# Kernel optimization log

Hardware: AMD Instinct MI355X
Metric: run time of the kernel (lower is better)

The kernel has to match this reference:

```python
import jax, jax.numpy as jnp
import numpy as np

DIM = 4096
BATCH = 8192
LAYERS = int(np.log2(DIM))  # 12


def _butterfly_indices(dim):
    lefts, rights = [], []
    for l in range(int(np.log2(dim))):
        stride = 1 << l
        starts = np.arange(0, dim, 2 * stride)[:, None]
        offs = np.arange(stride)[None, :]
        left = (starts + offs).reshape(-1)
        lefts.append(left)
        rights.append(left + stride)
    return np.stack(lefts), np.stack(rights)  # (layers, dim//2)


def setup_inputs() -> dict:
    key = jax.random.key(0)
    kx, ka = jax.random.split(key)
    x = jax.random.normal(kx, (BATCH, DIM), dtype=jnp.float32)
    # angles ~ Uniform(-0.05, 0.05), one per pair per layer
    angles = jax.random.uniform(ka, (LAYERS, DIM // 2), dtype=jnp.float32,
                                minval=-0.05, maxval=0.05)
    li, ri = _butterfly_indices(DIM)
    left_idx = jnp.asarray(li, dtype=jnp.int64) if jax.config.jax_enable_x64 else jnp.asarray(li, dtype=jnp.int32)
    right_idx = jnp.asarray(ri, dtype=left_idx.dtype)
    return {"x": x, "angles": angles, "left_idx": left_idx, "right_idx": right_idx}


def reference(x, angles, left_idx, right_idx):
    # x: (B, D); angles/left_idx/right_idx: (layers, D//2)
    y = x
    for l in range(angles.shape[0]):  # fixed small loop over log2(D) layers
        c = jnp.cos(angles[l])  # (D//2,)
        s = jnp.sin(angles[l])
        xl = jnp.take(y, left_idx[l], axis=1)   # (B, D//2)
        xr = jnpp_take(y, right_idx[l]) if False else jnp.take(y, right_idx[l], axis=1)
        new_left = xl * c + xr * s
        new_right = -xl * s + xr * c
        # left/right indices partition [0, D), so the scatter fully overwrites y
        y = jnp.zeros_like(y).at[:, left_idx[l]].set(new_left).at[:, right_idx[l]].set(new_right)
    return y
```

## Files before the change

kernel.cpp:

```cpp
#include <hip/hip_runtime.h>
#include <cmath>


namespace {
constexpr int kDim = 4096;
constexpr int kBatch = 8192;
constexpr int kLayers = 12;
constexpr int kPairs = kDim / 2;
constexpr int kRowsPerBlock = 2;
constexpr int kThreads = 256;
constexpr int kLdsWords = kDim + 4 * (kDim / 64);
}

__device__ __forceinline__ int lds_pad(int i) { return i + ((i >> 6) << 2); }

__device__ __forceinline__ int slot_to_pair(int l, int t, int q) {
    const int m = l & 3;
    const int phase = l >> 2;
    const int j = ((q >> m) << (m + 1)) | (q & ((1 << m) - 1));
    int i;
    if (phase == 0)      i = 16 * t + j;
    else if (phase == 1) i = (t & 15) + 16 * j + 256 * (t >> 4);
    else                 i = t + 256 * j;
    const int s = 1 << l;
    return ((i >> (l + 1)) << l) | (i & (s - 1));
}

__global__ void bf_precompute_cs(const float* __restrict__ angles,
                                 float* __restrict__ cperm,
                                 float* __restrict__ sperm) {
    const int k = blockIdx.x * blockDim.x + threadIdx.x;
    if (k >= kLayers * kPairs) return;
    const int l = k >> 11;
    const int slot = k & 2047;
    const int t = slot >> 3;
    const int q = slot & 7;
    const int p = slot_to_pair(l, t, q);
    const float a = angles[l * kPairs + p];
    float sv, cv;
    sincosf(a, &sv, &cv);
    cperm[k] = cv;
    sperm[k] = sv;
}

template <int PHASE>
__device__ __forceinline__ void apply_phase(float (&v)[kRowsPerBlock][16], int t,
                                            const float* __restrict__ cperm,
                                            const float* __restrict__ sperm) {
#pragma unroll
    for (int m = 0; m < 4; ++m) {
        const int l = PHASE * 4 + m;
        const float4* cp = reinterpret_cast<const float4*>(cperm + l * kPairs + 8 * t);
        const float4* sp = reinterpret_cast<const float4*>(sperm + l * kPairs + 8 * t);
        const float4 c0 = cp[0], c1 = cp[1];
        const float4 s0 = sp[0], s1 = sp[1];
        const float c[8] = {c0.x, c0.y, c0.z, c0.w, c1.x, c1.y, c1.z, c1.w};
        const float s[8] = {s0.x, s0.y, s0.z, s0.w, s1.x, s1.y, s1.z, s1.w};
#pragma unroll
        for (int q = 0; q < 8; ++q) {
            const int j = ((q >> m) << (m + 1)) | (q & ((1 << m) - 1));
            const int jp = j + (1 << m);
#pragma unroll
            for (int r = 0; r < kRowsPerBlock; ++r) {
                const float xl = v[r][j], xr = v[r][jp];
                v[r][j]  = fmaf(xl, c[q],  xr * s[q]);
                v[r][jp] = fmaf(xr, c[q], -xl * s[q]);
            }
        }
    }
}

__global__ __launch_bounds__(kThreads, 4)
void bf_butterfly(const float* __restrict__ x,
                  const float* __restrict__ cperm,
                  const float* __restrict__ sperm,
                  float* __restrict__ out) {
    __shared__ float lds[kRowsPerBlock][kLdsWords];
    const int t = threadIdx.x;
    const int row0 = blockIdx.x * kRowsPerBlock;

    float v[kRowsPerBlock][16];

#pragma unroll
    for (int r = 0; r < kRowsPerBlock; ++r) {
        const float4* src = reinterpret_cast<const float4*>(
            x + (size_t)(row0 + r) * kDim + 16 * t);
#pragma unroll
        for (int k = 0; k < 4; ++k) {
            const float4 f = src[k];
            v[r][4 * k + 0] = f.x; v[r][4 * k + 1] = f.y;
            v[r][4 * k + 2] = f.z; v[r][4 * k + 3] = f.w;
        }
    }

    apply_phase<0>(v, t, cperm, sperm);

#pragma unroll
    for (int r = 0; r < kRowsPerBlock; ++r) {
#pragma unroll
        for (int k = 0; k < 4; ++k) {
            *reinterpret_cast<float4*>(&lds[r][lds_pad(16 * t + 4 * k)]) =
                make_float4(v[r][4 * k], v[r][4 * k + 1], v[r][4 * k + 2], v[r][4 * k + 3]);
        }
    }
    __syncthreads();
    const int low = t & 15, high = t >> 4;
#pragma unroll
    for (int r = 0; r < kRowsPerBlock; ++r) {
#pragma unroll
        for (int j = 0; j < 16; ++j) {
            v[r][j] = lds[r][lds_pad(low + 16 * j + 256 * high)];
        }
    }

    apply_phase<1>(v, t, cperm, sperm);

    __syncthreads();
#pragma unroll
    for (int r = 0; r < kRowsPerBlock; ++r) {
#pragma unroll
        for (int j = 0; j < 16; ++j) {
            lds[r][lds_pad(low + 16 * j + 256 * high)] = v[r][j];
        }
    }
    __syncthreads();
#pragma unroll
    for (int r = 0; r < kRowsPerBlock; ++r) {
#pragma unroll
        for (int j = 0; j < 16; ++j) {
            v[r][j] = lds[r][lds_pad(t + 256 * j)];
        }
    }

    apply_phase<2>(v, t, cperm, sperm);

#pragma unroll
    for (int r = 0; r < kRowsPerBlock; ++r) {
        float* dst = out + (size_t)(row0 + r) * kDim;
#pragma unroll
        for (int j = 0; j < 16; ++j) {
            dst[t + 256 * j] = v[r][j];
        }
    }
}

extern "C" void kernel_launch(void* const* d_in, const int* in_sizes, int n_in,
                              void* d_out, int out_size, void* d_ws, size_t ws_size,
                              hipStream_t stream) {
    (void)in_sizes; (void)n_in; (void)out_size; (void)ws_size;
    const float* x = (const float*)d_in[0];
    const float* angles = (const float*)d_in[1];
    float* cperm = (float*)d_ws;
    float* sperm = cperm + kLayers * kPairs;
    float* out = (float*)d_out;

    bf_precompute_cs<<<(kLayers * kPairs + kThreads - 1) / kThreads, kThreads, 0, stream>>>(
        angles, cperm, sperm);
    bf_butterfly<<<kBatch / kRowsPerBlock, kThreads, 0, stream>>>(x, cperm, sperm, out);
}
```

Baseline: 251.7 us.

## Pack cos/sin as fp16 half2 and process one row per block

Stores the rotation coefficients as a packed half2 (cos-1, sin) instead of two fp32 arrays, which halves coefficient load traffic and instruction count per layer. It also drops to one row per block with a higher occupancy hint, so there are more, smaller blocks. This loses the coefficient reuse across two rows and adds half-to-float conversions. Using fp16 for sin and cos-1 adds a small precision loss in the coefficients.

Result: slower. 271.8 us (+8.0%).

```diff
diff --git a/kernel.cpp b/kernel.cpp
--- a/kernel.cpp
+++ b/kernel.cpp
@@ -1,4 +1,5 @@
 #include <hip/hip_runtime.h>
+#include <hip/hip_fp16.h>
 #include <cmath>
 
 
@@ -7,7 +8,6 @@
 constexpr int kBatch = 8192;
 constexpr int kLayers = 12;
 constexpr int kPairs = kDim / 2;
-constexpr int kRowsPerBlock = 2;
 constexpr int kThreads = 256;
 constexpr int kLdsWords = kDim + 4 * (kDim / 64);
 }
@@ -27,8 +27,7 @@
 }
 
 __global__ void bf_precompute_cs(const float* __restrict__ angles,
-                                 float* __restrict__ cperm,
-                                 float* __restrict__ sperm) {
+                                 __half2* __restrict__ csperm) {
     const int k = blockIdx.x * blockDim.x + threadIdx.x;
     if (k >= kLayers * kPairs) return;
     const int l = k >> 11;
@@ -39,108 +38,85 @@
     const float a = angles[l * kPairs + p];
     float sv, cv;
     sincosf(a, &sv, &cv);
-    cperm[k] = cv;
-    sperm[k] = sv;
+    csperm[k] = __floats2half2_rn(cv - 1.0f, sv);
 }
 
 template <int PHASE>
-__device__ __forceinline__ void apply_phase(float (&v)[kRowsPerBlock][16], int t,
-                                            const float* __restrict__ cperm,
-                                            const float* __restrict__ sperm) {
+__device__ __forceinline__ void apply_phase(float (&v)[16], int t,
+                                            const __half2* __restrict__ csperm) {
 #pragma unroll
     for (int m = 0; m < 4; ++m) {
         const int l = PHASE * 4 + m;
-        const float4* cp = reinterpret_cast<const float4*>(cperm + l * kPairs + 8 * t);
-        const float4* sp = reinterpret_cast<const float4*>(sperm + l * kPairs + 8 * t);
-        const float4 c0 = cp[0], c1 = cp[1];
-        const float4 s0 = sp[0], s1 = sp[1];
-        const float c[8] = {c0.x, c0.y, c0.z, c0.w, c1.x, c1.y, c1.z, c1.w};
-        const float s[8] = {s0.x, s0.y, s0.z, s0.w, s1.x, s1.y, s1.z, s1.w};
+        const uint4* pp = reinterpret_cast<const uint4*>(csperm + l * kPairs + 8 * t);
+        const uint4 p0 = pp[0], p1 = pp[1];
+        __half2 h[8];
+        *reinterpret_cast<uint4*>(&h[0]) = p0;
+        *reinterpret_cast<uint4*>(&h[4]) = p1;
 #pragma unroll
         for (int q = 0; q < 8; ++q) {
             const int j = ((q >> m) << (m + 1)) | (q & ((1 << m) - 1));
             const int jp = j + (1 << m);
-#pragma unroll
-            for (int r = 0; r < kRowsPerBlock; ++r) {
-                const float xl = v[r][j], xr = v[r][jp];
-                v[r][j]  = fmaf(xl, c[q],  xr * s[q]);
-                v[r][jp] = fmaf(xr, c[q], -xl * s[q]);
-            }
+            const float2 f = __half22float2(h[q]);
+            const float c = 1.0f + f.x;
+            const float s = f.y;
+            const float xl = v[j], xr = v[jp];
+            v[j]  = fmaf(xl, c,  xr * s);
+            v[jp] = fmaf(xr, c, -xl * s);
         }
     }
 }
 
-__global__ __launch_bounds__(kThreads, 4)
+__global__ __launch_bounds__(kThreads, 8)
 void bf_butterfly(const float* __restrict__ x,
-                  const float* __restrict__ cperm,
-                  const float* __restrict__ sperm,
+                  const __half2* __restrict__ csperm,
                   float* __restrict__ out) {
-    __shared__ float lds[kRowsPerBlock][kLdsWords];
+    __shared__ float lds[kLdsWords];
     const int t = threadIdx.x;
-    const int row0 = blockIdx.x * kRowsPerBlock;
+    const int row = blockIdx.x;
 
-    float v[kRowsPerBlock][16];
+    float v[16];
+
+    const float4* src = reinterpret_cast<const float4*>(x + (size_t)row * kDim + 16 * t);
+#pragma unroll
+    for (int k = 0; k < 4; ++k) {
+        const float4 f = src[k];
+        v[4 * k + 0] = f.x; v[4 * k + 1] = f.y;
+        v[4 * k + 2] = f.z; v[4 * k + 3] = f.w;
+    }
+
+    apply_phase<0>(v, t, csperm);
 
 #pragma unroll
-    for (int r = 0; r < kRowsPerBlock; ++r) {
-        const float4* src = reinterpret_cast<const float4*>(
-            x + (size_t)(row0 + r) * kDim + 16 * t);
-#pragma unroll
-        for (int k = 0; k < 4; ++k) {
-            const float4 f = src[k];
-            v[r][4 * k + 0] = f.x; v[r][4 * k + 1] = f.y;
-            v[r][4 * k + 2] = f.z; v[r][4 * k + 3] = f.w;
-        }
-    }
-
-    apply_phase<0>(v, t, cperm, sperm);
-
-#pragma unroll
-    for (int r = 0; r < kRowsPerBlock; ++r) {
-#pragma unroll
-        for (int k = 0; k < 4; ++k) {
-            *reinterpret_cast<float4*>(&lds[r][lds_pad(16 * t + 4 * k)]) =
-                make_float4(v[r][4 * k], v[r][4 * k + 1], v[r][4 * k + 2], v[r][4 * k + 3]);
-        }
+    for (int k = 0; k < 4; ++k) {
+        *reinterpret_cast<float4*>(&lds[lds_pad(16 * t + 4 * k)]) =
+            make_float4(v[4 * k], v[4 * k + 1], v[4 * k + 2], v[4 * k + 3]);
     }
     __syncthreads();
     const int low = t & 15, high = t >> 4;
 #pragma unroll
-    for (int r = 0; r < kRowsPerBlock; ++r) {
-#pragma unroll
-        for (int j = 0; j < 16; ++j) {
-            v[r][j] = lds[r][lds_pad(low + 16 * j + 256 * high)];
-        }
+    for (int j = 0; j < 16; ++j) {
+        v[j] = lds[lds_pad(low + 16 * j + 256 * high)];
     }
 
-    apply_phase<1>(v, t, cperm, sperm);
+    apply_phase<1>(v, t, csperm);
 
     __syncthreads();
 #pragma unroll
-    for (int r = 0; r < kRowsPerBlock; ++r) {
-#pragma unroll
-        for (int j = 0; j < 16; ++j) {
-            lds[r][lds_pad(low + 16 * j + 256 * high)] = v[r][j];
-        }
+    for (int j = 0; j < 16; ++j) {
+        lds[lds_pad(low + 16 * j + 256 * high)] = v[j];
     }
     __syncthreads();
 #pragma unroll
-    for (int r = 0; r < kRowsPerBlock; ++r) {
-#pragma unroll
-        for (int j = 0; j < 16; ++j) {
-            v[r][j] = lds[r][lds_pad(t + 256 * j)];
-        }
+    for (int j = 0; j < 16; ++j) {
+        v[j] = lds[lds_pad(t + 256 * j)];
     }
 
-    apply_phase<2>(v, t, cperm, sperm);
+    apply_phase<2>(v, t, csperm);
 
+    float* dst = out + (size_t)row * kDim;
 #pragma unroll
-    for (int r = 0; r < kRowsPerBlock; ++r) {
-        float* dst = out + (size_t)(row0 + r) * kDim;
-#pragma unroll
-        for (int j = 0; j < 16; ++j) {
-            dst[t + 256 * j] = v[r][j];
-        }
+    for (int j = 0; j < 16; ++j) {
+        dst[t + 256 * j] = v[j];
     }
 }
 
@@ -150,11 +126,10 @@
     (void)in_sizes; (void)n_in; (void)out_size; (void)ws_size;
     const float* x = (const float*)d_in[0];
     const float* angles = (const float*)d_in[1];
-    float* cperm = (float*)d_ws;
-    float* sperm = cperm + kLayers * kPairs;
+    __half2* csperm = (__half2*)d_ws;
     float* out = (float*)d_out;
 
     bf_precompute_cs<<<(kLayers * kPairs + kThreads - 1) / kThreads, kThreads, 0, stream>>>(
-        angles, cperm, sperm);
-    bf_butterfly<<<kBatch / kRowsPerBlock, kThreads, 0, stream>>>(x, cperm, sperm, out);
+        angles, csperm);
+    bf_butterfly<<<kBatch, kThreads, 0, stream>>>(x, csperm, out);
 }
```
